# Kernel tuning notes

Measured on AMD Instinct MI355X. Metric: run time of the kernel, lower is better.

The kernel has to match this reference:

```python
import jax, jax.numpy as jnp
import numpy as np
from jax import lax

B, C, TX, TY = 16, 192, 512, 2048
SEG = 8192 // 256  # segment_frames = 32 (hop length 256)
NEG_INF = -1e9


def setup_inputs() -> dict:
    key = jax.random.key(0)
    ks = jax.random.split(key, 7)
    z = jax.random.normal(ks[0], (B, C, TY), jnp.float32)
    z_p = jax.random.normal(ks[1], (B, C, TY), jnp.float32)
    m_p = jax.random.normal(ks[2], (B, C, TX), jnp.float32)
    logs_p = 0.1 * jax.random.normal(ks[3], (B, C, TX), jnp.float32)
    x_lengths = jax.random.randint(ks[4], (B,), TX // 2, TX + 1, jnp.int32)
    y_lengths = jax.random.randint(ks[5], (B,), TY // 2, TY + 1, jnp.int32)
    rand_u = jax.random.uniform(ks[6], (B,), jnp.float32)
    return dict(z=z, z_p=z_p, m_p=m_p, logs_p=logs_p,
                x_lengths=x_lengths, y_lengths=y_lengths, rand_u=rand_u)


def neg_cent_fn(z_p, m_p, logs_p):
    # sum_c -0.5 * exp(-2 logs)[c,tx] * (z_p[c,ty] - m_p[c,tx])^2 - sum_c logs[c,tx]
    # expanded (z-m)^2 = z^2 - 2 z m + m^2 -> batched GEMMs (same math as broadcast form)
    s = jnp.exp(-2.0 * logs_p)                                 # [B,C,Tx]
    a = jnp.einsum('bct,bcs->bts', -0.5 * z_p * z_p, s)        # [B,Ty,Tx]
    b = jnp.einsum('bct,bcs->bts', z_p, s * m_p)               # [B,Ty,Tx]
    c = jnp.sum(-0.5 * s * m_p * m_p - logs_p, axis=1)         # [B,Tx]
    return a + b + c[:, None, :]


def maximum_path_single(value, t_x, t_y):
    # Monotonic alignment search DP on value [Ty,Tx], valid region [:t_y,:t_x].
    Ty, Tx = value.shape
    tx = jnp.arange(Tx)

    def fwd(v, row):
        v_shift = jnp.concatenate([jnp.full((1,), NEG_INF, v.dtype), v[:-1]])
        dirn = v_shift > v                      # True: best predecessor is tx-1
        v_new = row + jnp.maximum(v, v_shift)
        v_new = jnp.where(tx < t_x, v_new, NEG_INF)
        v_new = jnp.maximum(v_new, NEG_INF)     # clamp accumulation
        return v_new, dirn

    v0 = jnp.where(tx == 0, 0.0, NEG_INF)
    _, dirs = lax.scan(fwd, v0, value)          # dirs [Ty,Tx] bool

    def bwd(idx, j):
        active = j < t_y
        idx = jnp.where(j == t_y - 1, t_x - 1, idx)
        row = jnp.where(active, jnp.zeros((Tx,), value.dtype).at[idx].set(1.0), 0.0)
        idx = jnp.where(active, idx - dirs[j, idx].astype(idx.dtype), idx)
        return idx, row

    _, path_rev = lax.scan(bwd, jnp.int32(0), jnp.arange(Ty - 1, -1, -1))
    return path_rev[::-1]                       # [Ty,Tx] 0/1 path


def rand_slice_segments(z, y_lengths, rand_u):
    t = z.shape[2]
    safe = jnp.minimum(y_lengths, t)
    ids_max = jnp.maximum(safe - SEG, 0)
    ids = (rand_u * (ids_max.astype(jnp.float32) + 1e-8)).astype(jnp.int32)
    zs = jax.vmap(lambda zi, s: lax.dynamic_slice_in_dim(zi, s, SEG, axis=1))(z, ids)
    valid = (jnp.arange(SEG)[None, None, :] < (safe - ids)[:, None, None])
    return zs * valid.astype(z.dtype), ids


def reference(z, z_p, m_p, logs_p, x_lengths, y_lengths, rand_u):
    neg_cent = neg_cent_fn(z_p, m_p, logs_p)                     # [B,Ty,Tx]
    attn = jax.vmap(maximum_path_single)(neg_cent, x_lengths, y_lengths)
    attn = lax.stop_gradient(attn)                               # torch: no_grad + detach
    m_p_a = jnp.einsum('bts,bcs->bct', attn, m_p)                # [B,C,Ty]
    logs_p_a = jnp.einsum('bts,bcs->bct', attn, logs_p)          # [B,C,Ty]
    z_slice, ids_slice = rand_slice_segments(z, y_lengths, rand_u)
    return z_slice, ids_slice, attn, m_p_a, logs_p_a
```

## Files before the change

### kernel.cpp

```cpp
#include <hip/hip_runtime.h>
#include <stdint.h>

#define B_   16
#define C_   192
#define TX_  512
#define TY_  2048
#define K_   384
#define SEG_ 32
#define NEG_INF_ (-1e9f)

#define NPROD_ 8
#define NSLOT_ 8


__global__ __launch_bounds__(128) void k_prep(const float* __restrict__ mp,
                                              const float* __restrict__ logsp,
                                              float* __restrict__ Bmat,
                                              float* __restrict__ cterm) {
    int b  = blockIdx.y;
    int tx = blockIdx.x * 128 + threadIdx.x;
    const float* mb = mp    + (size_t)b * C_ * TX_ + tx;
    const float* lb = logsp + (size_t)b * C_ * TX_ + tx;
    float* B0 = Bmat + (size_t)b * K_ * TX_ + tx;
    float acc = 0.f;
    for (int c = 0; c < C_; ++c) {
        float lg = lb[(size_t)c * TX_];
        float m  = mb[(size_t)c * TX_];
        float s  = expf(-2.f * lg);
        B0[(size_t)c * TX_]        = s;
        B0[(size_t)(C_ + c) * TX_] = s * m;
        acc += -0.5f * s * m * m - lg;
    }
    cterm[b * TX_ + tx] = acc;
}

__global__ __launch_bounds__(256) void k_gemm(const float* __restrict__ zp,
                                              const float* __restrict__ Bmat,
                                              const float* __restrict__ cterm,
                                              float* __restrict__ ncout) {
    __shared__ float As[16][128];
    __shared__ float Bs[16][128];
    int b  = blockIdx.z;
    int m0 = blockIdx.y * 128;
    int n0 = blockIdx.x * 128;
    int tid = threadIdx.x;
    int tm = tid >> 4;
    int tn = tid & 15;
    const float* zpb = zp   + (size_t)b * C_ * TY_;
    const float* Bb  = Bmat + (size_t)b * K_ * TX_;

    float acc[8][8];
#pragma unroll
    for (int i = 0; i < 8; ++i)
#pragma unroll
        for (int j = 0; j < 8; ++j) acc[i][j] = 0.f;

    int lrow = tid >> 5;
    int lcol = (tid & 31) << 2;

    for (int k0 = 0; k0 < K_; k0 += 16) {
        int ksrc = (k0 < C_) ? k0 : (k0 - C_);
        const float* Ab = zpb + (size_t)(ksrc + lrow) * TY_ + m0 + lcol;
        float4 z0 = *(const float4*)Ab;
        float4 z1 = *(const float4*)(Ab + (size_t)8 * TY_);
        if (k0 < C_) {
            z0.x = -0.5f * z0.x * z0.x; z0.y = -0.5f * z0.y * z0.y;
            z0.z = -0.5f * z0.z * z0.z; z0.w = -0.5f * z0.w * z0.w;
            z1.x = -0.5f * z1.x * z1.x; z1.y = -0.5f * z1.y * z1.y;
            z1.z = -0.5f * z1.z * z1.z; z1.w = -0.5f * z1.w * z1.w;
        }
        const float* Bp = Bb + (size_t)(k0 + lrow) * TX_ + n0 + lcol;
        float4 w0 = *(const float4*)Bp;
        float4 w1 = *(const float4*)(Bp + (size_t)8 * TX_);

        __syncthreads();
        *(float4*)&As[lrow][lcol]     = z0;
        *(float4*)&As[lrow + 8][lcol] = z1;
        *(float4*)&Bs[lrow][lcol]     = w0;
        *(float4*)&Bs[lrow + 8][lcol] = w1;
        __syncthreads();

#pragma unroll
        for (int kk = 0; kk < 16; ++kk) {
            float4 a0 = *(const float4*)&As[kk][tm * 8];
            float4 a1 = *(const float4*)&As[kk][tm * 8 + 4];
            float4 b0 = *(const float4*)&Bs[kk][tn * 8];
            float4 b1 = *(const float4*)&Bs[kk][tn * 8 + 4];
            float a[8]  = {a0.x, a0.y, a0.z, a0.w, a1.x, a1.y, a1.z, a1.w};
            float bb[8] = {b0.x, b0.y, b0.z, b0.w, b1.x, b1.y, b1.z, b1.w};
#pragma unroll
            for (int i = 0; i < 8; ++i)
#pragma unroll
                for (int j = 0; j < 8; ++j)
                    acc[i][j] = fmaf(a[i], bb[j], acc[i][j]);
        }
    }

    float cadd[8];
#pragma unroll
    for (int j = 0; j < 8; ++j) cadd[j] = cterm[b * TX_ + n0 + tn * 8 + j];

#pragma unroll
    for (int i = 0; i < 8; ++i) {
        int row = m0 + tm * 8 + i;
        float* orow = ncout + ((size_t)b * TY_ + row) * TX_ + n0 + tn * 8;
        float4 o0, o1;
        o0.x = acc[i][0] + cadd[0]; o0.y = acc[i][1] + cadd[1];
        o0.z = acc[i][2] + cadd[2]; o0.w = acc[i][3] + cadd[3];
        o1.x = acc[i][4] + cadd[4]; o1.y = acc[i][5] + cadd[5];
        o1.z = acc[i][6] + cadd[6]; o1.w = acc[i][7] + cadd[7];
        *(float4*)orow       = o0;
        *(float4*)(orow + 4) = o1;
    }
}

#if __has_builtin(__builtin_amdgcn_update_dpp)
#define LEFT_OF(v7)                                                          \
    __int_as_float(__builtin_amdgcn_update_dpp(                              \
        __float_as_int(NEG_INF_), __float_as_int(v7), 0x138, 0xF, 0xF, false))
#else
#define LEFT_OF(v7)                                                          \
    ({ float _l = __shfl_up((v7), 1); if (lane == 0) _l = NEG_INF_; _l; })
#endif

__global__ __launch_bounds__(576, 1) void k_dp(const float* __restrict__ nc,
                                               const int* __restrict__ xl,
                                               const int* __restrict__ yl,
                                               int* __restrict__ path,
                                               int* __restrict__ gdirs) {
    extern __shared__ unsigned char sdirs[];
    float*    stage   = (float*)sdirs;
    volatile int* vpf = (volatile int*)(sdirs + 131072);
    volatile int* vcf = (volatile int*)(sdirs + 131072 + 64);
    int b    = blockIdx.x;
    int tid  = threadIdx.x;
    int wid  = tid >> 6;
    int lane = tid & 63;
    int t_x  = xl[b];
    int t_y  = yl[b]; if (t_y > TY_) t_y = TY_;
    const float* ncb = nc + (size_t)b * TY_ * TX_;
    int* gd32 = gdirs + b * (TY_ * 64 / 4);

    int ng = (t_y + 7) >> 3;

    if (tid < NSLOT_) vpf[tid] = -1;
    if (tid == NSLOT_) vcf[0] = -1;
    __syncthreads();

    if (wid == 0) {
        int col0 = lane * 8;
        float v[8];
#pragma unroll
        for (int k = 0; k < 8; ++k) v[k] = (col0 + k == 0) ? 0.f : NEG_INF_;

        for (int g = 0; g < ng; ++g) {
            int slot = g & (NSLOT_ - 1);
            int spin = 0;
            bool lds_ok = true;
            while (vpf[slot] != g) {
                if (++spin > 4096) { lds_ok = false; break; }
            }
            __builtin_amdgcn_sched_barrier(0);

            float4 q[16];
            if (lds_ok) {
                const float* lb = stage + slot * 4096 + lane * 4;
#pragma unroll
                for (int r = 0; r < 8; ++r) {
                    q[2 * r]     = *(const float4*)(lb + r * 512);
                    q[2 * r + 1] = *(const float4*)(lb + r * 512 + 256);
                }
            } else {
                const float* gp = ncb + (size_t)g * 8 * TX_ + lane * 8;
#pragma unroll
                for (int r = 0; r < 8; ++r) {
                    q[2 * r]     = *(const float4*)(gp + (size_t)r * TX_);
                    q[2 * r + 1] = *(const float4*)(gp + (size_t)r * TX_ + 4);
                }
            }

            unsigned dw0 = 0u, dw1 = 0u;
#pragma unroll
            for (int r = 0; r < 8; ++r) {
                float rc[8] = {q[2 * r].x,     q[2 * r].y,
                               q[2 * r].z,     q[2 * r].w,
                               q[2 * r + 1].x, q[2 * r + 1].y,
                               q[2 * r + 1].z, q[2 * r + 1].w};
                float left = LEFT_OF(v[7]);
                unsigned by = 0u;
#pragma unroll
                for (int k = 7; k >= 0; --k) {
                    float vs = (k == 0) ? left : v[k - 1];
                    if (vs > v[k]) by |= (1u << k);
                    v[k] = fmaxf(v[k], vs) + rc[k];
                }
                if (r < 4) dw0 |= by << (8 * r);
                else       dw1 |= by << (8 * (r - 4));
            }
            gd32[(2 * g)     * 64 + lane] = (int)dw0;
            gd32[(2 * g + 1) * 64 + lane] = (int)dw1;
            asm volatile("s_waitcnt lgkmcnt(0)" ::: "memory");
            __builtin_amdgcn_sched_barrier(0);
            if (lane == 0) vcf[0] = g;
        }
    } else {
        int w = wid - 1;
        float* lb = stage + w * 4096 + lane * 4;
        bool alive = true;
        for (int g = w; alive && g < ng; g += NPROD_) {
            int spin = 0;
            while (vcf[0] < g - NSLOT_) {
                __builtin_amdgcn_s_sleep(2);
                if (++spin > (1 << 14)) { alive = false; break; }
            }
            if (!alive) break;
            __builtin_amdgcn_sched_barrier(0);
            const float* gp = ncb + (size_t)g * 8 * TX_ + lane * 8;
            float4 q[8], p[8];
#pragma unroll
            for (int r = 0; r < 8; ++r) {
                q[r] = *(const float4*)(gp + (size_t)r * TX_);
                p[r] = *(const float4*)(gp + (size_t)r * TX_ + 4);
            }
#pragma unroll
            for (int r = 0; r < 8; ++r) {
                *(float4*)(lb + r * 512)       = q[r];
                *(float4*)(lb + r * 512 + 256) = p[r];
            }
            __threadfence_block();
            if (lane == 0) vpf[w] = g;
        }
    }

    __syncthreads();

    {
        const float4* g4 = (const float4*)gd32;
        float4* s4 = (float4*)sdirs;
        for (int i = tid; i < TY_ * 16 / 4; i += 576) s4[i] = g4[i];
    }
    __syncthreads();

    int* pb = path + b * TY_;
    for (int j = t_y + tid; j < TY_; j += 576) pb[j] = -1;

    if (tid == 0) {
        int idx = t_x - 1;
        int j   = t_y - 1;
        while (j >= 0) {
            int n  = (j + 1 < 8) ? (j + 1) : 8;
            int bs = (idx - 7) >> 3; if (bs < 0) bs = 0;
            int b2 = bs + 1;         if (b2 > 63) b2 = 63;
            unsigned lo[8], hi[8];
#pragma unroll
            for (int r = 0; r < 8; ++r) {
                if (r < n) {
                    int jr = j - r;
                    int rb = (jr >> 2) * 256 + (jr & 3);
                    lo[r] = sdirs[rb + bs * 4];
                    hi[r] = sdirs[rb + b2 * 4];
                }
            }
#pragma unroll
            for (int r = 0; r < 8; ++r) {
                if (r < n) {
                    pb[j - r] = idx;
                    int Bi = idx >> 3;
                    unsigned byte = (Bi == bs) ? lo[r] : hi[r];
                    idx -= (int)((byte >> (idx & 7)) & 1u);
                }
            }
            j -= n;
        }
    }
}

__global__ __launch_bounds__(256) void k_attn(const int* __restrict__ path,
                                              float* __restrict__ attn) {
    int i   = blockIdx.x * 256 + threadIdx.x;
    int tx0 = (i & 127) << 2;
    int bty = i >> 7;
    int p   = path[bty];
    float4 o;
    o.x = (p == tx0)     ? 1.f : 0.f;
    o.y = (p == tx0 + 1) ? 1.f : 0.f;
    o.z = (p == tx0 + 2) ? 1.f : 0.f;
    o.w = (p == tx0 + 3) ? 1.f : 0.f;
    ((float4*)attn)[i] = o;
}

__global__ __launch_bounds__(256) void k_proj(const int* __restrict__ path,
                                              const float* __restrict__ mp,
                                              const float* __restrict__ logsp,
                                              float* __restrict__ mpa,
                                              float* __restrict__ logsa) {
    int i   = blockIdx.x * 256 + threadIdx.x;
    int ty0 = (i & 511) << 2;
    int bc  = i >> 9;
    int b   = bc / C_;
    const int4 p4 = *(const int4*)(path + b * TY_ + ty0);
    const float* mrow = mp    + (size_t)bc * TX_;
    const float* lrow = logsp + (size_t)bc * TX_;
    float4 mo, lo;
    mo.x = (p4.x >= 0) ? mrow[p4.x] : 0.f;  lo.x = (p4.x >= 0) ? lrow[p4.x] : 0.f;
    mo.y = (p4.y >= 0) ? mrow[p4.y] : 0.f;  lo.y = (p4.y >= 0) ? lrow[p4.y] : 0.f;
    mo.z = (p4.z >= 0) ? mrow[p4.z] : 0.f;  lo.z = (p4.z >= 0) ? lrow[p4.z] : 0.f;
    mo.w = (p4.w >= 0) ? mrow[p4.w] : 0.f;  lo.w = (p4.w >= 0) ? lrow[p4.w] : 0.f;
    ((float4*)mpa)[i]   = mo;
    ((float4*)logsa)[i] = lo;
}

__global__ __launch_bounds__(256) void k_slice(const float* __restrict__ z,
                                               const int* __restrict__ yl,
                                               const float* __restrict__ ru,
                                               float* __restrict__ zs,
                                               float* __restrict__ oid) {
    int b = blockIdx.x;
    int safe = yl[b]; if (safe > TY_) safe = TY_;
    int idsmax = safe - SEG_; if (idsmax < 0) idsmax = 0;
    int ids = (int)(ru[b] * ((float)idsmax + 1e-8f));
    int lim = safe - ids;
    for (int t = threadIdx.x; t < C_ * SEG_; t += 256) {
        int c = t >> 5, k = t & 31;
        zs[b * C_ * SEG_ + t] =
            (k < lim) ? z[((size_t)b * C_ + c) * TY_ + ids + k] : 0.f;
    }
    if (threadIdx.x == 0) oid[b] = (float)ids;
}

extern "C" void kernel_launch(void* const* d_in, const int* in_sizes, int n_in,
                              void* d_out, int out_size, void* d_ws, size_t ws_size,
                              hipStream_t stream) {
    const float* z     = (const float*)d_in[0];
    const float* zp    = (const float*)d_in[1];
    const float* mp    = (const float*)d_in[2];
    const float* logsp = (const float*)d_in[3];
    const int*   xl    = (const int*)d_in[4];
    const int*   yl    = (const int*)d_in[5];
    const float* ru    = (const float*)d_in[6];

    float* out     = (float*)d_out;
    float* o_zs    = out;
    float* o_ids   = out + 98304;
    float* o_attn  = out + 98320;
    float* o_mpa   = out + 16875536;
    float* o_logsa = out + 23166992;

    float* Bmat  = (float*)d_ws;
    float* cterm = Bmat + (size_t)B_ * K_ * TX_;
    int*   path  = (int*)(cterm + B_ * TX_);
    int*   gdirs = (int*)o_mpa;

    hipFuncSetAttribute((const void*)k_dp,
                        hipFuncAttributeMaxDynamicSharedMemorySize,
                        TY_ * 64 + 256);

    hipLaunchKernelGGL(k_prep, dim3(TX_ / 128, B_), dim3(128), 0, stream,
                       mp, logsp, Bmat, cterm);
    hipLaunchKernelGGL(k_gemm, dim3(TX_ / 128, TY_ / 128, B_), dim3(256), 0, stream,
                       zp, Bmat, cterm, o_attn);
    hipLaunchKernelGGL(k_dp, dim3(B_), dim3(576), TY_ * 64 + 256, stream,
                       o_attn, xl, yl, path, gdirs);
    hipLaunchKernelGGL(k_attn, dim3(B_ * TY_ * TX_ / 4 / 256), dim3(256), 0, stream,
                       path, o_attn);
    hipLaunchKernelGGL(k_proj, dim3(B_ * C_ * TY_ / 4 / 256), dim3(256), 0, stream,
                       path, mp, logsp, o_mpa, o_logsa);
    hipLaunchKernelGGL(k_slice, dim3(B_), dim3(256), 0, stream,
                       z, yl, ru, o_zs, o_ids);
}
```

Measured before the change: 776.6 us.

## Replace spin-flag producer/consumer in DP kernel with barrier double-buffering

The DP kernel previously used per-slot volatile LDS flags, with eight producer waves spinning and sleeping to feed the single DP wave through an 8-slot ring. It now stages 32 rows per step into two LDS halves. Producer waves prefetch the next 32-row super-group while wave 0 runs the DP on the current one, and each step is separated by __syncthreads. This removes the spin-polling, the sleep latency and the global-memory fallback path. In exchange, every super-group now pays a block barrier, and producers can only run one stage ahead instead of eight.

```diff
diff --git a/kernel.cpp b/kernel.cpp
--- a/kernel.cpp
+++ b/kernel.cpp
@@ -8,9 +8,6 @@
 #define K_   384
 #define SEG_ 32
 #define NEG_INF_ (-1e9f)
-
-#define NPROD_ 8
-#define NSLOT_ 8
 
 
 __global__ __launch_bounds__(128) void k_prep(const float* __restrict__ mp,
@@ -129,9 +126,7 @@
                                                int* __restrict__ path,
                                                int* __restrict__ gdirs) {
     extern __shared__ unsigned char sdirs[];
-    float*    stage   = (float*)sdirs;
-    volatile int* vpf = (volatile int*)(sdirs + 131072);
-    volatile int* vcf = (volatile int*)(sdirs + 131072 + 64);
+    float* stage = (float*)sdirs;
     int b    = blockIdx.x;
     int tid  = threadIdx.x;
     int wid  = tid >> 6;
@@ -141,94 +136,79 @@
     const float* ncb = nc + (size_t)b * TY_ * TX_;
     int* gd32 = gdirs + b * (TY_ * 64 / 4);
 
-    int ng = (t_y + 7) >> 3;
-
-    if (tid < NSLOT_) vpf[tid] = -1;
-    if (tid == NSLOT_) vcf[0] = -1;
-    __syncthreads();
-
-    if (wid == 0) {
+    int nsg = (t_y + 31) >> 5;
+
+    if (wid > 0) {
+        int w = wid - 1;
+        float* lb = stage + (4 * w) * 512 + lane * 4;
+        const float* gp = ncb + (size_t)(4 * w) * TX_ + lane * 8;
+#pragma unroll
+        for (int r = 0; r < 4; ++r) {
+            float4 a = *(const float4*)(gp + (size_t)r * TX_);
+            float4 c = *(const float4*)(gp + (size_t)r * TX_ + 4);
+            *(float4*)(lb + r * 512)       = a;
+            *(float4*)(lb + r * 512 + 256) = c;
+        }
+    }
+
+    float v[8];
+    {
         int col0 = lane * 8;
-        float v[8];
 #pragma unroll
         for (int k = 0; k < 8; ++k) v[k] = (col0 + k == 0) ? 0.f : NEG_INF_;
-
-        for (int g = 0; g < ng; ++g) {
-            int slot = g & (NSLOT_ - 1);
-            int spin = 0;
-            bool lds_ok = true;
-            while (vpf[slot] != g) {
-                if (++spin > 4096) { lds_ok = false; break; }
+    }
+
+    for (int sg = 0; sg < nsg; ++sg) {
+        __syncthreads();
+
+        if (wid > 0) {
+            int sgn = sg + 1;
+            if (sgn < nsg) {
+                int w = wid - 1;
+                int row0 = sgn * 32 + 4 * w;
+                float* lb = stage + ((sgn & 1) * 16384) + (4 * w) * 512 + lane * 4;
+                const float* gp = ncb + (size_t)row0 * TX_ + lane * 8;
+#pragma unroll
+                for (int r = 0; r < 4; ++r) {
+                    float4 a = *(const float4*)(gp + (size_t)r * TX_);
+                    float4 c = *(const float4*)(gp + (size_t)r * TX_ + 4);
+                    *(float4*)(lb + r * 512)       = a;
+                    *(float4*)(lb + r * 512 + 256) = c;
+                }
             }
-            __builtin_amdgcn_sched_barrier(0);
-
-            float4 q[16];
-            if (lds_ok) {
-                const float* lb = stage + slot * 4096 + lane * 4;
+        } else {
+            const float* half = stage + (sg & 1) * 16384 + lane * 4;
+            for (int r8 = 0; r8 < 4; ++r8) {
+                if (sg * 32 + r8 * 8 >= t_y) break;
+                const float* lb = half + r8 * 4096;
+                float4 q[16];
 #pragma unroll
                 for (int r = 0; r < 8; ++r) {
                     q[2 * r]     = *(const float4*)(lb + r * 512);
                     q[2 * r + 1] = *(const float4*)(lb + r * 512 + 256);
                 }
-            } else {
-                const float* gp = ncb + (size_t)g * 8 * TX_ + lane * 8;
+                unsigned dw0 = 0u, dw1 = 0u;
 #pragma unroll
                 for (int r = 0; r < 8; ++r) {
-                    q[2 * r]     = *(const float4*)(gp + (size_t)r * TX_);
-                    q[2 * r + 1] = *(const float4*)(gp + (size_t)r * TX_ + 4);
-                }
+                    float rc[8] = {q[2 * r].x,     q[2 * r].y,
+                                   q[2 * r].z,     q[2 * r].w,
+                                   q[2 * r + 1].x, q[2 * r + 1].y,
+                                   q[2 * r + 1].z, q[2 * r + 1].w};
+                    float left = LEFT_OF(v[7]);
+                    unsigned by = 0u;
+#pragma unroll
+                    for (int k = 7; k >= 0; --k) {
+                        float vs = (k == 0) ? left : v[k - 1];
+                        if (vs > v[k]) by |= (1u << k);
+                        v[k] = fmaxf(v[k], vs) + rc[k];
+                    }
+                    if (r < 4) dw0 |= by << (8 * r);
+                    else       dw1 |= by << (8 * (r - 4));
+                }
+                int g = sg * 4 + r8;
+                gd32[(2 * g)     * 64 + lane] = (int)dw0;
+                gd32[(2 * g + 1) * 64 + lane] = (int)dw1;
             }
-
-            unsigned dw0 = 0u, dw1 = 0u;
-#pragma unroll
-            for (int r = 0; r < 8; ++r) {
-                float rc[8] = {q[2 * r].x,     q[2 * r].y,
-                               q[2 * r].z,     q[2 * r].w,
-                               q[2 * r + 1].x, q[2 * r + 1].y,
-                               q[2 * r + 1].z, q[2 * r + 1].w};
-                float left = LEFT_OF(v[7]);
-                unsigned by = 0u;
-#pragma unroll
-                for (int k = 7; k >= 0; --k) {
-                    float vs = (k == 0) ? left : v[k - 1];
-                    if (vs > v[k]) by |= (1u << k);
-                    v[k] = fmaxf(v[k], vs) + rc[k];
-                }
-                if (r < 4) dw0 |= by << (8 * r);
-                else       dw1 |= by << (8 * (r - 4));
-            }
-            gd32[(2 * g)     * 64 + lane] = (int)dw0;
-            gd32[(2 * g + 1) * 64 + lane] = (int)dw1;
-            asm volatile("s_waitcnt lgkmcnt(0)" ::: "memory");
-            __builtin_amdgcn_sched_barrier(0);
-            if (lane == 0) vcf[0] = g;
-        }
-    } else {
-        int w = wid - 1;
-        float* lb = stage + w * 4096 + lane * 4;
-        bool alive = true;
-        for (int g = w; alive && g < ng; g += NPROD_) {
-            int spin = 0;
-            while (vcf[0] < g - NSLOT_) {
-                __builtin_amdgcn_s_sleep(2);
-                if (++spin > (1 << 14)) { alive = false; break; }
-            }
-            if (!alive) break;
-            __builtin_amdgcn_sched_barrier(0);
-            const float* gp = ncb + (size_t)g * 8 * TX_ + lane * 8;
-            float4 q[8], p[8];
-#pragma unroll
-            for (int r = 0; r < 8; ++r) {
-                q[r] = *(const float4*)(gp + (size_t)r * TX_);
-                p[r] = *(const float4*)(gp + (size_t)r * TX_ + 4);
-            }
-#pragma unroll
-            for (int r = 0; r < 8; ++r) {
-                *(float4*)(lb + r * 512)       = q[r];
-                *(float4*)(lb + r * 512 + 256) = p[r];
-            }
-            __threadfence_block();
-            if (lane == 0) vpf[w] = g;
         }
     }
 
@@ -353,13 +333,13 @@
 
     hipFuncSetAttribute((const void*)k_dp,
                         hipFuncAttributeMaxDynamicSharedMemorySize,
-                        TY_ * 64 + 256);
+                        TY_ * 64);
 
     hipLaunchKernelGGL(k_prep, dim3(TX_ / 128, B_), dim3(128), 0, stream,
                        mp, logsp, Bmat, cterm);
     hipLaunchKernelGGL(k_gemm, dim3(TX_ / 128, TY_ / 128, B_), dim3(256), 0, stream,
                        zp, Bmat, cterm, o_attn);
-    hipLaunchKernelGGL(k_dp, dim3(B_), dim3(576), TY_ * 64 + 256, stream,
+    hipLaunchKernelGGL(k_dp, dim3(B_), dim3(576), TY_ * 64, stream,
                        o_attn, xl, yl, path, gdirs);
     hipLaunchKernelGGL(k_attn, dim3(B_ * TY_ * TX_ / 4 / 256), dim3(256), 0, stream,
                        path, o_attn);
```

Measured after the change: 741.3 us. 1.05x faster.
